# Kernel tuning notes

Measured on AMD Instinct MI355X. Metric: run time of the kernel, lower is better.

Reference implementation:

```python
import jax, jax.numpy as jnp
import numpy as np

MASK_LOGIT_CONST = 1000000000.0
LN_EPS = 1e-12


def setup_inputs() -> dict:
    key = jax.random.key(0)
    k_in, k_w = jax.random.split(key)
    B, S, H = 8, 2048, 1024
    inputs = jax.random.normal(k_in, (B, S, H), dtype=jnp.float32)
    masks = jnp.ones((B, S, S), dtype=jnp.float32)
    w_match = jax.random.normal(k_w, (2 * H, H), dtype=jnp.float32) * (1.0 / np.sqrt(2 * H))
    b_match = jnp.zeros((H,), dtype=jnp.float32)
    ln_gamma = jnp.ones((H,), dtype=jnp.float32)
    ln_beta = jnp.zeros((H,), dtype=jnp.float32)
    return {"inputs": inputs, "masks": masks, "w_match": w_match,
            "b_match": b_match, "ln_gamma": ln_gamma, "ln_beta": ln_beta}


def reference(inputs, masks, w_match, b_match, ln_gamma, ln_beta):
    H = inputs.shape[-1]
    scale = 1.0 / jnp.sqrt(jnp.asarray(H, dtype=inputs.dtype))
    # self-attention scores [B,S,S] (dropout disabled -> query=key=inputs)
    scores = jnp.einsum('bsh,bth->bst', inputs, inputs) * scale
    # logits_mask: scores*mask + (-C)*(1-mask)
    scores = scores * masks - MASK_LOGIT_CONST * (1.0 - masks)
    probs = jax.nn.softmax(scores, axis=-1)
    context = jnp.einsum('bst,bth->bsh', probs, inputs)
    cat = jnp.concatenate([inputs, context], axis=-1)  # [B,S,2H]
    matching = jnp.einsum('bsk,kh->bsh', cat, w_match) + b_match
    # layernorm over last dim
    mu = jnp.mean(matching, axis=-1, keepdims=True)
    var = jnp.mean((matching - mu) ** 2, axis=-1, keepdims=True)
    normed = (matching - mu) * jax.lax.rsqrt(var + LN_EPS)
    return normed * ln_gamma + ln_beta
```

## Files before the change

### kernel.cpp

```cpp
#include <hip/hip_runtime.h>
#include <hip/hip_bf16.h>
#include <hip/hip_fp8.h>


typedef unsigned short ushort_t;
typedef __attribute__((ext_vector_type(8))) short short8;
typedef __attribute__((ext_vector_type(4))) float float4v;

__device__ inline float b2f(unsigned int u) {
    union { unsigned int i; float f; } v; v.i = u << 16; return v.f;
}
__device__ inline ushort_t f2b(float f) {
    __hip_bfloat16 h = __float2bfloat16(f);
    return __builtin_bit_cast(ushort_t, h);
}
__device__ inline unsigned char f2e4(float f) {
    return __hip_fp8_e4m3(f).__x;
}

__device__ inline void gload_lds16(const void* g, void* lds) {
    __builtin_amdgcn_global_load_lds(
        (const __attribute__((address_space(1))) unsigned int*)g,
        (__attribute__((address_space(3))) unsigned int*)lds, 16, 0, 0);
}

template<int EPI>
__global__ __launch_bounds__(512, 2)
void gemm_bt(const ushort_t* __restrict__ A, const ushort_t* __restrict__ A2, int kSplit,
             const ushort_t* __restrict__ B,
             int M, int N, int K, int lda, int ldb, int ldc,
             long aBS, long bBS, long cBS,
             const float* __restrict__ bias,
             ushort_t* __restrict__ outb)
{
    __shared__ __align__(16) ushort_t smem[4 * 16384];

    const int tid = threadIdx.x;
    const int z = blockIdx.z;
    A  += (size_t)z * aBS;
    A2 += (size_t)z * aBS;
    B  += (size_t)z * bBS;
    outb += (size_t)z * cBS;

    const int bm = blockIdx.x * 256;
    const int bn = blockIdx.y * 256;
    const int w = tid >> 6, lane = tid & 63;
    const int wm = (w >> 2) * 128, wn = (w & 3) * 64;
    const int q = lane >> 4, l15 = lane & 15;
    const int srow = lane >> 2;
    const int schunk = ((lane & 3) ^ ((lane >> 3) & 3)) * 8;

    float4v acc[8][4];
#pragma unroll
    for (int i = 0; i < 8; i++)
#pragma unroll
        for (int j = 0; j < 4; j++) acc[i][j] = (float4v){0.f, 0.f, 0.f, 0.f};

    float rsum0 = 0.f, rsum1 = 0.f;

    const int NT = K >> 5;

#define STAGE(T) do {                                                               \
        const int k0_ = (T) * 32;                                                   \
        const ushort_t* aS_ = A; int ka_ = k0_;                                     \
        if (k0_ >= kSplit) { aS_ = A2; ka_ = k0_ - kSplit; }                        \
        ushort_t* buf_ = &smem[((T) & 3) * 16384];                                  \
        gload_lds16(aS_ + (size_t)(bm + w * 16       + srow) * lda + ka_ + schunk,  \
                    buf_ + w * 512);                                                \
        gload_lds16(aS_ + (size_t)(bm + (w + 8) * 16 + srow) * lda + ka_ + schunk,  \
                    buf_ + (w + 8) * 512);                                          \
        gload_lds16(B   + (size_t)(bn + w * 16       + srow) * ldb + k0_ + schunk,  \
                    buf_ + 8192 + w * 512);                                         \
        gload_lds16(B   + (size_t)(bn + (w + 8) * 16 + srow) * ldb + k0_ + schunk,  \
                    buf_ + 8192 + (w + 8) * 512);                                   \
    } while (0)

    STAGE(0); STAGE(1); STAGE(2);

    for (int T = 0; T < NT; ++T) {
        if (T + 2 < NT)      asm volatile("s_waitcnt vmcnt(8)\n\ts_barrier" ::: "memory");
        else if (T + 1 < NT) asm volatile("s_waitcnt vmcnt(4)\n\ts_barrier" ::: "memory");
        else                 asm volatile("s_waitcnt vmcnt(0)\n\ts_barrier" ::: "memory");

        if (T + 3 < NT) STAGE(T + 3);

        const ushort_t* bufA = &smem[(T & 3) * 16384];
        const ushort_t* bufB = bufA + 8192;
        short8 af[8], bf[4];
#pragma unroll
        for (int mi = 0; mi < 8; mi++) {
            const int r = wm + mi * 16 + l15;
            af[mi] = *(const short8*)(&bufA[r * 32 + ((q ^ ((r >> 1) & 3)) << 3)]);
            if (EPI == 2 && (mi >> 1) == (w & 3)) {
                float s8 = 0.f;
#pragma unroll
                for (int e = 0; e < 8; e++) s8 += b2f((ushort_t)af[mi][e]);
                if (mi & 1) rsum1 += s8; else rsum0 += s8;
            }
        }
#pragma unroll
        for (int ni = 0; ni < 4; ni++) {
            const int r = wn + ni * 16 + l15;
            bf[ni] = *(const short8*)(&bufB[r * 32 + ((q ^ ((r >> 1) & 3)) << 3)]);
        }
        __builtin_amdgcn_s_setprio(1);
#pragma unroll
        for (int mi = 0; mi < 8; mi++)
#pragma unroll
            for (int ni = 0; ni < 4; ni++)
                acc[mi][ni] = __builtin_amdgcn_mfma_f32_16x16x32_bf16(
                    af[mi], bf[ni], acc[mi][ni], 0, 0, 0);
        __builtin_amdgcn_s_setprio(0);
    }
#undef STAGE

    float* rsld = (float*)smem;
    if (EPI == 2) {
        rsum0 += __shfl_xor(rsum0, 16); rsum0 += __shfl_xor(rsum0, 32);
        rsum1 += __shfl_xor(rsum1, 16); rsum1 += __shfl_xor(rsum1, 32);
        if (lane < 16) {
            const int m0 = 2 * (w & 3);
            rsld[wm + m0 * 16 + l15]       = rsum0;
            rsld[wm + (m0 + 1) * 16 + l15] = rsum1;
        }
        __syncthreads();
    }

#pragma unroll
    for (int mi = 0; mi < 8; mi++) {
#pragma unroll
        for (int r = 0; r < 4; r++) {
            const int row = bm + wm + mi * 16 + q * 4 + r;
            const size_t ro = (size_t)row * ldc;
            float rsinv = 1.f;
            if (EPI == 2) rsinv = 1.0f / rsld[wm + mi * 16 + q * 4 + r];
#pragma unroll
            for (int ni = 0; ni < 4; ni++) {
                const int col = bn + wn + ni * 16 + l15;
                float v = acc[mi][ni][r];
                if (EPI == 2) outb[ro + col] = f2b(v * rsinv);
                else          outb[ro + col] = f2b(v + bias[col]);
            }
        }
    }
}

__global__ __launch_bounds__(256, 2)
void gemm1_fp8(const unsigned char* __restrict__ X8,
               const float* __restrict__ mask,
               ushort_t* __restrict__ E)
{
    __shared__ __align__(16) unsigned char As[128 * 128];
    __shared__ __align__(16) unsigned char Bs[128 * 128];

    const int tid = threadIdx.x;
    const int z = blockIdx.z;
    const unsigned char* Xz = X8 + (size_t)z * 2048 * 1024;
    const float* mz = mask + (size_t)z * 2048 * 2048;
    ushort_t* Ez = E + (size_t)z * 2048 * 2048;

    const int bm = blockIdx.x * 128;
    const int bn = blockIdx.y * 128;
    const int wave = tid >> 6, lane = tid & 63;
    const int wm = (wave >> 1) * 64, wn = (wave & 1) * 64;
    const int q = lane >> 4, l15 = lane & 15;
    const int rx = l15 & 7;
    const int lrow = lane >> 3;
    const int cswz = (lane & 7) ^ lrow;

    float4v acc[4][4];
#pragma unroll
    for (int i = 0; i < 4; i++)
#pragma unroll
        for (int j = 0; j < 4; j++) acc[i][j] = (float4v){0.f, 0.f, 0.f, 0.f};

    for (int k0 = 0; k0 < 1024; k0 += 128) {
#pragma unroll
        for (int j = 0; j < 4; j++) {
            const int p = wave * 4 + j;
            const int ro = p * 8 + lrow;
            gload_lds16(Xz + (size_t)(bm + ro) * 1024 + k0 + cswz * 16, &As[p * 1024]);
            gload_lds16(Xz + (size_t)(bn + ro) * 1024 + k0 + cswz * 16, &Bs[p * 1024]);
        }
        __syncthreads();
#pragma unroll
        for (int kk = 0; kk < 128; kk += 32) {
            const int g = (kk >> 3) + q;
            const int co = (((g >> 1) ^ rx) << 4) + ((g & 1) << 3);
            long af[4], bfv[4];
#pragma unroll
            for (int mi = 0; mi < 4; mi++)
                af[mi] = *(const long*)(&As[(wm + mi * 16 + l15) * 128 + co]);
#pragma unroll
            for (int ni = 0; ni < 4; ni++)
                bfv[ni] = *(const long*)(&Bs[(wn + ni * 16 + l15) * 128 + co]);
#pragma unroll
            for (int mi = 0; mi < 4; mi++)
#pragma unroll
                for (int ni = 0; ni < 4; ni++)
                    acc[mi][ni] = __builtin_amdgcn_mfma_f32_16x16x32_fp8_fp8(
                        af[mi], bfv[ni], acc[mi][ni], 0, 0, 0);
        }
        __syncthreads();
    }

    const float scale = 0.03125f;
#pragma unroll
    for (int mi = 0; mi < 4; mi++) {
#pragma unroll
        for (int r = 0; r < 4; r++) {
            const int row = bm + wm + mi * 16 + q * 4 + r;
            const size_t ro = (size_t)row * 2048;
#pragma unroll
            for (int ni = 0; ni < 4; ni++) {
                const int col = bn + wn + ni * 16 + l15;
                const float m = mz[ro + col];
                float v = __expf(acc[mi][ni][r] * scale * m - 1e9f * (1.0f - m));
                Ez[ro + col] = f2b(v);
            }
        }
    }
}

__global__ __launch_bounds__(256)
void conv_trans(const float* __restrict__ in, ushort_t* __restrict__ outT,
                ushort_t* __restrict__ outS, unsigned char* __restrict__ outQ,
                const float* __restrict__ inW, ushort_t* __restrict__ outTW,
                int R, int C)
{
    __shared__ float tile[64][65];
    const int tx = threadIdx.x & 15, ty = threadIdx.x >> 4;
    const int z = blockIdx.z;
    const float* src;
    ushort_t* dstT; ushort_t* dstS; unsigned char* dstQ;
    if (z == 8) {
        src = inW; dstT = outTW; dstS = nullptr; dstQ = nullptr;
    } else {
        const size_t zoff = (size_t)z * R * C;
        src = in + zoff; dstT = outT + zoff;
        dstS = outS + zoff; dstQ = outQ + zoff;
    }
    const int r0 = blockIdx.y * 64, c0 = blockIdx.x * 64;
#pragma unroll
    for (int j = 0; j < 4; j++) {
        const int r = ty + j * 16;
        const float4 v = *(const float4*)(src + (size_t)(r0 + r) * C + c0 + tx * 4);
        tile[r][tx * 4 + 0] = v.x;
        tile[r][tx * 4 + 1] = v.y;
        tile[r][tx * 4 + 2] = v.z;
        tile[r][tx * 4 + 3] = v.w;
        if (dstS) {
            ushort4 o;
            o.x = f2b(v.x); o.y = f2b(v.y); o.z = f2b(v.z); o.w = f2b(v.w);
            *(ushort4*)(dstS + (size_t)(r0 + r) * C + c0 + tx * 4) = o;
            uchar4 p;
            p.x = f2e4(v.x); p.y = f2e4(v.y); p.z = f2e4(v.z); p.w = f2e4(v.w);
            *(uchar4*)(dstQ + (size_t)(r0 + r) * C + c0 + tx * 4) = p;
        }
    }
    __syncthreads();
#pragma unroll
    for (int j = 0; j < 4; j++) {
        const int cc = ty + j * 16;
        ushort4 o;
        o.x = f2b(tile[tx * 4 + 0][cc]);
        o.y = f2b(tile[tx * 4 + 1][cc]);
        o.z = f2b(tile[tx * 4 + 2][cc]);
        o.w = f2b(tile[tx * 4 + 3][cc]);
        *(ushort4*)(dstT + (size_t)(c0 + cc) * R + r0 + tx * 4) = o;
    }
}

__global__ __launch_bounds__(256)
void ln_k(const ushort_t* __restrict__ Mt, const float* __restrict__ gamma,
          const float* __restrict__ beta, float* __restrict__ out)
{
    const size_t row = blockIdx.x;
    const int tid = threadIdx.x;
    const ushort4 u = *(const ushort4*)(Mt + row * 1024 + tid * 4);
    float x0 = b2f(u.x), x1 = b2f(u.y), x2 = b2f(u.z), x3 = b2f(u.w);
    float s  = x0 + x1 + x2 + x3;
    float s2 = x0 * x0 + x1 * x1 + x2 * x2 + x3 * x3;
#pragma unroll
    for (int off = 32; off > 0; off >>= 1) {
        s  += __shfl_down(s, off);
        s2 += __shfl_down(s2, off);
    }
    __shared__ float red[8];
    const int wave = tid >> 6, lane = tid & 63;
    if (lane == 0) { red[wave] = s; red[4 + wave] = s2; }
    __syncthreads();
    s  = red[0] + red[1] + red[2] + red[3];
    s2 = red[4] + red[5] + red[6] + red[7];
    const float mu  = s * (1.0f / 1024.0f);
    const float var = s2 * (1.0f / 1024.0f) - mu * mu;
    const float rinv = rsqrtf(var + 1e-12f);
    const float4 g = *(const float4*)(gamma + tid * 4);
    const float4 b = *(const float4*)(beta + tid * 4);
    float4 o;
    o.x = (x0 - mu) * rinv * g.x + b.x;
    o.y = (x1 - mu) * rinv * g.y + b.y;
    o.z = (x2 - mu) * rinv * g.z + b.z;
    o.w = (x3 - mu) * rinv * g.w + b.w;
    *(float4*)(out + row * 1024 + tid * 4) = o;
}

extern "C" void kernel_launch(void* const* d_in, const int* in_sizes, int n_in,
                              void* d_out, int out_size, void* d_ws, size_t ws_size,
                              hipStream_t stream)
{
    const float* X     = (const float*)d_in[0];
    const float* masks = (const float*)d_in[1];
    const float* Wm    = (const float*)d_in[2];
    const float* bias  = (const float*)d_in[3];
    const float* gamma = (const float*)d_in[4];
    const float* beta  = (const float*)d_in[5];
    float* out = (float*)d_out;
    char* ws = (char*)d_ws;

    const int B = 8, S = 2048, H = 1024;

    ushort_t* Xb  = (ushort_t*)(ws);
    ushort_t* XT  = (ushort_t*)(ws + 33554432);
    ushort_t* WT  = (ushort_t*)(ws + 67108864);
    ushort_t* E   = (ushort_t*)(ws + 71303168);
    ushort_t* CTX = (ushort_t*)(ws + 138477568);
    unsigned char* X8 = (unsigned char*)CTX;
    ushort_t* matching = E;

    conv_trans<<<dim3(16, 32, 9), 256, 0, stream>>>(X, XT, Xb, X8, Wm, WT, S, H);

    gemm1_fp8<<<dim3(16, 16, 8), 256, 0, stream>>>(X8, masks, E);

    gemm_bt<2><<<dim3(8, 4, 8), 512, 0, stream>>>(
        E, E, 1 << 30, XT,
        S, H, S, S, S, H,
        (long)S * S, (long)H * S, (long)S * H,
        nullptr, CTX);

    gemm_bt<3><<<dim3(64, 4, 1), 512, 0, stream>>>(
        Xb, CTX, H, WT,
        B * S, H, 2 * H, H, 2 * H, H,
        0, 0, 0,
        bias, matching);

    ln_k<<<B * S, 256, 0, stream>>>(matching, gamma, beta, out);
}
```

Baseline: 473.1 us.

## Halve K tile in fp8 score GEMM, use 16-byte LDS fragment reads and setprio

The QK^T fp8 GEMM now stages 64-wide K slices instead of 128, halving LDS use per block. It uses a new XOR swizzle so each lane reads one 16-byte vector covering two MFMA k-steps instead of separate 8-byte loads. It also wraps the MFMA block in s_setprio. This cuts LDS footprint and LDS instruction count, at the cost of twice as many loop iterations and barriers over K.

After: 485.1 us. +2.5%, slower.

```diff
diff --git a/kernel.cpp b/kernel.cpp
--- a/kernel.cpp
+++ b/kernel.cpp
@@ -6,6 +6,7 @@
 typedef unsigned short ushort_t;
 typedef __attribute__((ext_vector_type(8))) short short8;
 typedef __attribute__((ext_vector_type(4))) float float4v;
+typedef __attribute__((ext_vector_type(2))) long long2v;
 
 __device__ inline float b2f(unsigned int u) {
     union { unsigned int i; float f; } v; v.i = u << 16; return v.f;
@@ -150,8 +151,8 @@
                const float* __restrict__ mask,
                ushort_t* __restrict__ E)
 {
-    __shared__ __align__(16) unsigned char As[128 * 128];
-    __shared__ __align__(16) unsigned char Bs[128 * 128];
+    __shared__ __align__(16) unsigned char As[128 * 64];
+    __shared__ __align__(16) unsigned char Bs[128 * 64];
 
     const int tid = threadIdx.x;
     const int z = blockIdx.z;
@@ -164,9 +165,8 @@
     const int wave = tid >> 6, lane = tid & 63;
     const int wm = (wave >> 1) * 64, wn = (wave & 1) * 64;
     const int q = lane >> 4, l15 = lane & 15;
-    const int rx = l15 & 7;
-    const int lrow = lane >> 3;
-    const int cswz = (lane & 7) ^ lrow;
+    const int trow = tid >> 2;
+    const int sch = ((tid & 3) ^ ((tid >> 3) & 3)) * 16;
 
     float4v acc[4][4];
 #pragma unroll
@@ -174,33 +174,34 @@
 #pragma unroll
         for (int j = 0; j < 4; j++) acc[i][j] = (float4v){0.f, 0.f, 0.f, 0.f};
 
-    for (int k0 = 0; k0 < 1024; k0 += 128) {
-#pragma unroll
-        for (int j = 0; j < 4; j++) {
-            const int p = wave * 4 + j;
-            const int ro = p * 8 + lrow;
-            gload_lds16(Xz + (size_t)(bm + ro) * 1024 + k0 + cswz * 16, &As[p * 1024]);
-            gload_lds16(Xz + (size_t)(bn + ro) * 1024 + k0 + cswz * 16, &Bs[p * 1024]);
-        }
+    for (int k0 = 0; k0 < 1024; k0 += 64) {
+        gload_lds16(Xz + (size_t)(bm + trow) * 1024 + k0 + sch,      As + wave * 1024);
+        gload_lds16(Xz + (size_t)(bm + 64 + trow) * 1024 + k0 + sch, As + 4096 + wave * 1024);
+        gload_lds16(Xz + (size_t)(bn + trow) * 1024 + k0 + sch,      Bs + wave * 1024);
+        gload_lds16(Xz + (size_t)(bn + 64 + trow) * 1024 + k0 + sch, Bs + 4096 + wave * 1024);
         __syncthreads();
-#pragma unroll
-        for (int kk = 0; kk < 128; kk += 32) {
-            const int g = (kk >> 3) + q;
-            const int co = (((g >> 1) ^ rx) << 4) + ((g & 1) << 3);
-            long af[4], bfv[4];
-#pragma unroll
-            for (int mi = 0; mi < 4; mi++)
-                af[mi] = *(const long*)(&As[(wm + mi * 16 + l15) * 128 + co]);
-#pragma unroll
-            for (int ni = 0; ni < 4; ni++)
-                bfv[ni] = *(const long*)(&Bs[(wn + ni * 16 + l15) * 128 + co]);
+
+        long2v af[4], bfv[4];
+#pragma unroll
+        for (int mi = 0; mi < 4; mi++) {
+            const int r = wm + mi * 16 + l15;
+            af[mi] = *(const long2v*)(&As[r * 64 + ((q ^ ((r >> 1) & 3)) << 4)]);
+        }
+#pragma unroll
+        for (int ni = 0; ni < 4; ni++) {
+            const int r = wn + ni * 16 + l15;
+            bfv[ni] = *(const long2v*)(&Bs[r * 64 + ((q ^ ((r >> 1) & 3)) << 4)]);
+        }
+        __builtin_amdgcn_s_setprio(1);
+#pragma unroll
+        for (int s = 0; s < 2; s++)
 #pragma unroll
             for (int mi = 0; mi < 4; mi++)
 #pragma unroll
                 for (int ni = 0; ni < 4; ni++)
                     acc[mi][ni] = __builtin_amdgcn_mfma_f32_16x16x32_fp8_fp8(
-                        af[mi], bfv[ni], acc[mi][ni], 0, 0, 0);
-        }
+                        af[mi][s], bfv[ni][s], acc[mi][ni], 0, 0, 0);
+        __builtin_amdgcn_s_setprio(0);
         __syncthreads();
     }
 
```
